# Kernel optimization log

Hardware: AMD Instinct MI355X
Metric: run time of the kernel (lower is better)

## Reference

```python
import jax, jax.numpy as jnp
import numpy as np

K = 8
D_IN = 300 + K   # 308
H = 100          # hidden size hardcoded throughout the module
N = 768          # num_words (words in one table)


def setup_inputs() -> dict:
    key = jax.random.key(0)
    ks = jax.random.split(key, 24)
    f32 = jnp.float32

    def rn(k, shape, scale=0.05):
        return jax.random.normal(k, shape, dtype=f32) * scale

    inp = {
        'vv': jax.random.normal(ks[0], (N, D_IN), dtype=f32),
        'indices': jax.random.randint(ks[1], (N, 5), 0, N),
        'indices_not_found': jax.random.randint(ks[2], (N,), 0, 2).astype(bool),
        'num_words': N,
        # ModuleA: Linear(308, 100) + tanh
        'A_W': rn(ks[3], (D_IN, H)), 'A_b': jnp.zeros((H,), f32),
        # ModuleB: consumes concat(ww[N,500], hh[N,100]) -> Linear(600,100)+tanh
        'B_W': rn(ks[4], (5 * H + H, H)), 'B_b': jnp.zeros((H,), f32),
        # ModuleB2(100,100,100): two heads, oo and new hidden hh
        'B2_Wo': rn(ks[5], (H, H)), 'B2_bo': jnp.zeros((H,), f32),
        'B2_Wh': rn(ks[6], (H, H)), 'B2_bh': jnp.zeros((H,), f32),
        # ModuleD(100,100)
        'D_W': rn(ks[7], (H, H)), 'D_b': jnp.zeros((H,), f32),
    }
    # Three ModuleAssociate2 heads (rows/cols/cells): pairwise 2-layer MLP
    # score(o_i, o_j) = Linear(H,2)(relu(Linear(2H,H)(concat(o_i,o_j))))
    for i, name in enumerate(['rows', 'cols', 'cells']):
        k1, k2 = jax.random.split(ks[8 + i])
        inp[name + '_W1'] = rn(k1, (2 * H, H))
        inp[name + '_b1'] = jnp.zeros((H,), f32)
        inp[name + '_W2'] = rn(k2, (H, 2))
        inp[name + '_b2'] = jnp.zeros((2,), f32)
    return inp


def _concat_neighbors(uu, indices, not_found):
    # gather 5 neighbor feature rows -> (N, 5*H); zero rows where not found
    y = uu[indices].reshape(indices.shape[0], 5 * uu.shape[1])  # (N,5,H)->(N,500)
    return jnp.where(not_found[:, None], 0.0, y)


def _associate(o, W1, b1, W2, b2):
    # pairwise MLP over all (i,j) pairs without materializing the 2H concat:
    # concat(o_i,o_j) @ W1 == o_i @ W1[:H] + o_j @ W1[H:]
    h = o.shape[1]
    hl = o @ W1[:h]   # (N,H)
    hr = o @ W1[h:]   # (N,H)
    hid = jax.nn.relu(hl[:, None, :] + hr[None, :, :] + b1)  # (N,N,H)
    return hid @ W2 + b2  # (N,N,2)


def reference(indices, indices_not_found, vv, num_words,
              A_W, A_b, B_W, B_b, B2_Wo, B2_bo, B2_Wh, B2_bh, D_W, D_b,
              rows_W1, rows_b1, rows_W2, rows_b2,
              cols_W1, cols_b1, cols_W2, cols_b2,
              cells_W1, cells_b1, cells_W2, cells_b2):
    iterations = 1
    uu = jnp.tanh(vv @ A_W + A_b)                 # ModuleA: (N,100)
    hh = jnp.zeros((num_words, H), vv.dtype)
    for _ in range(iterations):
        ww = _concat_neighbors(uu, indices, indices_not_found)  # (N,500)
        bb = jnp.tanh(jnp.concatenate([ww, hh], axis=1) @ B_W + B_b)  # ModuleB
        oo = jnp.tanh(bb @ B2_Wo + B2_bo)          # ModuleB2 output head
        hh = jnp.tanh(bb @ B2_Wh + B2_bh)          # ModuleB2 hidden head
        uu = jnp.tanh(hh @ D_W + D_b)              # ModuleD
    return (_associate(oo, rows_W1, rows_b1, rows_W2, rows_b2),
            _associate(oo, cols_W1, cols_b1, cols_W2, cols_b2),
            _associate(oo, cells_W1, cells_b1, cells_W2, cells_b2))
```

## Files before the change

kernel.cpp:

```cpp
#include <hip/hip_runtime.h>
#include <hip/hip_bf16.h>

#define NW   768
#define HID  100
#define DIN  308
#define RPB  2
#define TP   32
#define LDP  108

typedef const float* fp;

__global__ __launch_bounds__(512) void k_uu(fp vv, fp A_W, fp A_b,
                                            float* __restrict__ uu) {
    __shared__ float vs[RPB][DIN];
    __shared__ float part[4][RPB][128];
    const int i0 = blockIdx.x * RPB;
    for (int t = threadIdx.x; t < RPB * DIN; t += 512) {
        const int r = t / DIN, k = t % DIN;
        vs[r][k] = vv[(i0 + r) * DIN + k];
    }
    __syncthreads();
    const int c = threadIdx.x & 127;
    const int s = threadIdx.x >> 7;
    float a0 = 0.f, a1 = 0.f;
    if (c < HID) {
        const int k0 = s * 77;
#pragma unroll 11
        for (int k = k0; k < k0 + 77; ++k) {
            const float w = A_W[k * HID + c];
            a0 = fmaf(vs[0][k], w, a0);
            a1 = fmaf(vs[1][k], w, a1);
        }
    }
    part[s][0][c] = a0; part[s][1][c] = a1;
    __syncthreads();
    for (int t = threadIdx.x; t < RPB * HID; t += 512) {
        const int r = t / HID, cc = t % HID;
        float acc = A_b[cc];
#pragma unroll
        for (int s2 = 0; s2 < 4; ++s2) acc += part[s2][r][cc];
        uu[(i0 + r) * HID + cc] = tanhf(acc);
    }
}

__global__ __launch_bounds__(640) void k_fused(
    const float* __restrict__ uu, const int* __restrict__ indices,
    const int* __restrict__ nf,
    fp B_W, fp B_b, fp B2_Wo, fp B2_bo,
    fp W1r, fp b1r, fp W1c, fp b1c, fp W1e, fp b1e,
    float* __restrict__ hlhr) {
    __shared__ __align__(16) float ww[RPB][5 * HID];
    __shared__ float part[5][RPB][128];
    __shared__ __align__(16) float bbs[RPB][HID];
    __shared__ __align__(16) float oos[RPB][HID];
    __shared__ int flags[6];
    __shared__ int smode[2];

    if (threadIdx.x < 6) flags[threadIdx.x] = 0;
    __syncthreads();
    if (threadIdx.x < 192) {
        const int t = threadIdx.x;
        const unsigned vn = (unsigned)nf[t];
        if (vn > 1u) atomicOr(&flags[0], 1);
        if (vn & 0xFEFEFEFEu) atomicOr(&flags[1], 1);
        if ((t & 1) && vn) atomicOr(&flags[2], 1);
        if (!(t & 1) && vn) atomicOr(&flags[3], 1);
        const unsigned vi = (unsigned)indices[t];
        if ((t & 1) && vi) atomicOr(&flags[4], 1);
        if (!(t & 1) && vi) atomicOr(&flags[5], 1);
    }
    __syncthreads();
    if (threadIdx.x == 0) {
        int m = 0;
        if (!flags[1] && flags[0]) m = 1;
        else if (!flags[2] && flags[3]) m = 2;
        smode[0] = m;
        smode[1] = (!flags[4] && flags[5]) ? 1 : 0;
    }
    __syncthreads();
    const int mnf = smode[0], midx = smode[1];

    const int i0 = blockIdx.x * RPB;
    for (int t = threadIdx.x; t < RPB * 5 * HID; t += 640) {
        const int r = t / (5 * HID), u = t % (5 * HID);
        const int i = i0 + r;
        const bool notf = (mnf == 1) ? (((const unsigned char*)nf)[i] != 0)
                        : (mnf == 2) ? (nf[2 * i] != 0)
                                     : (nf[i] != 0);
        const int q = u / HID, cc = u % HID;
        int j = midx ? indices[2 * (i * 5 + q)] : indices[i * 5 + q];
        j = (j < 0) ? 0 : ((j >= NW) ? NW - 1 : j);
        ww[r][u] = notf ? 0.f : uu[j * HID + cc];
    }
    __syncthreads();

    const int c = threadIdx.x % 128;
    const int s = threadIdx.x / 128;

    {
        float a0 = 0.f, a1 = 0.f;
        if (c < HID) {
            const int k0 = s * 100;
#pragma unroll 5
            for (int k = k0; k < k0 + 100; k += 4) {
                const float4 w0 = *(const float4*)&ww[0][k];
                const float4 w1 = *(const float4*)&ww[1][k];
                const float b0 = B_W[(k + 0) * HID + c];
                const float b1v = B_W[(k + 1) * HID + c];
                const float b2v = B_W[(k + 2) * HID + c];
                const float b3 = B_W[(k + 3) * HID + c];
                a0 = fmaf(w0.x, b0, a0); a1 = fmaf(w1.x, b0, a1);
                a0 = fmaf(w0.y, b1v, a0); a1 = fmaf(w1.y, b1v, a1);
                a0 = fmaf(w0.z, b2v, a0); a1 = fmaf(w1.z, b2v, a1);
                a0 = fmaf(w0.w, b3, a0); a1 = fmaf(w1.w, b3, a1);
            }
        }
        part[s][0][c] = a0; part[s][1][c] = a1;
    }
    __syncthreads();
    for (int t = threadIdx.x; t < RPB * HID; t += 640) {
        const int r = t / HID, cc = t % HID;
        float acc = B_b[cc];
#pragma unroll
        for (int s2 = 0; s2 < 5; ++s2) acc += part[s2][r][cc];
        bbs[r][cc] = tanhf(acc);
    }
    __syncthreads();

    {
        float a0 = 0.f, a1 = 0.f;
        if (c < HID) {
            const int k0 = s * 20;
#pragma unroll 5
            for (int k = k0; k < k0 + 20; k += 4) {
                const float4 w0 = *(const float4*)&bbs[0][k];
                const float4 w1 = *(const float4*)&bbs[1][k];
                const float b0 = B2_Wo[(k + 0) * HID + c];
                const float b1v = B2_Wo[(k + 1) * HID + c];
                const float b2v = B2_Wo[(k + 2) * HID + c];
                const float b3 = B2_Wo[(k + 3) * HID + c];
                a0 = fmaf(w0.x, b0, a0); a1 = fmaf(w1.x, b0, a1);
                a0 = fmaf(w0.y, b1v, a0); a1 = fmaf(w1.y, b1v, a1);
                a0 = fmaf(w0.z, b2v, a0); a1 = fmaf(w1.z, b2v, a1);
                a0 = fmaf(w0.w, b3, a0); a1 = fmaf(w1.w, b3, a1);
            }
        }
        part[s][0][c] = a0; part[s][1][c] = a1;
    }
    __syncthreads();
    for (int t = threadIdx.x; t < RPB * HID; t += 640) {
        const int r = t / HID, cc = t % HID;
        float acc = B2_bo[cc];
#pragma unroll
        for (int s2 = 0; s2 < 5; ++s2) acc += part[s2][r][cc];
        oos[r][cc] = tanhf(acc);
    }
    __syncthreads();

    const int u = threadIdx.x;
    if (u < 600) {
        const int ho = u / HID;
        const int cc = u % HID;
        const int h = ho >> 1, half = ho & 1;
        fp W1 = (h == 0) ? W1r : ((h == 1) ? W1c : W1e);
        fp b1 = (h == 0) ? b1r : ((h == 1) ? b1c : b1e);
        const float bias = half ? 0.f : b1[cc];
        float a0 = bias, a1 = bias;
        const float* Wp = W1 + half * HID * HID;
#pragma unroll 5
        for (int k = 0; k < HID; k += 4) {
            const float4 o0 = *(const float4*)&oos[0][k];
            const float4 o1 = *(const float4*)&oos[1][k];
            const float b0 = Wp[(k + 0) * HID + cc];
            const float b1v = Wp[(k + 1) * HID + cc];
            const float b2v = Wp[(k + 2) * HID + cc];
            const float b3 = Wp[(k + 3) * HID + cc];
            a0 = fmaf(o0.x, b0, a0); a1 = fmaf(o1.x, b0, a1);
            a0 = fmaf(o0.y, b1v, a0); a1 = fmaf(o1.y, b1v, a1);
            a0 = fmaf(o0.z, b2v, a0); a1 = fmaf(o1.z, b2v, a1);
            a0 = fmaf(o0.w, b3, a0); a1 = fmaf(o1.w, b3, a1);
        }
        hlhr[(size_t)ho * (NW * HID) + (size_t)(i0 + 0) * HID + cc] = a0;
        hlhr[(size_t)ho * (NW * HID) + (size_t)(i0 + 1) * HID + cc] = a1;
    }
}

__global__ __launch_bounds__(256, 4) void k_pair(
    const float* __restrict__ hlhr,
    fp W2r, fp b2r, fp W2c, fp b2c, fp W2e, fp b2e,
    float* __restrict__ out) {
    __shared__ __align__(16) float hlS[TP][LDP];
    __shared__ __align__(16) float hrS[TP][LDP];
    __shared__ __align__(16) float w2a[HID];
    __shared__ __align__(16) float w2b[HID];

    const int h  = blockIdx.z;
    const int i0 = blockIdx.y * TP;
    const int j0 = blockIdx.x * TP;
    const float* hl = hlhr + (size_t)(h * 2 + 0) * (NW * HID) + (size_t)i0 * HID;
    const float* hr = hlhr + (size_t)(h * 2 + 1) * (NW * HID) + (size_t)j0 * HID;
    fp W2 = (h == 0) ? W2r : ((h == 1) ? W2c : W2e);
    fp b2 = (h == 0) ? b2r : ((h == 1) ? b2c : b2e);

    for (int t = threadIdx.x; t < TP * HID; t += 256) {
        const int r = t / HID, c = t % HID;
        hlS[r][c] = hl[t];
        hrS[r][c] = hr[t];
    }
    if (threadIdx.x < HID) {
        w2a[threadIdx.x] = W2[2 * threadIdx.x];
        w2b[threadIdx.x] = W2[2 * threadIdx.x + 1];
    }
    __syncthreads();

    const int tx = threadIdx.x & 15;
    const int ty = threadIdx.x >> 4;
    float acc0[2][2] = {};
    float acc1[2][2] = {};

#pragma unroll 5
    for (int kb = 0; kb < HID; kb += 4) {
        const float4 a0 = *(const float4*)&hlS[ty * 2 + 0][kb];
        const float4 a1 = *(const float4*)&hlS[ty * 2 + 1][kb];
        const float4 r0 = *(const float4*)&hrS[tx * 2 + 0][kb];
        const float4 r1 = *(const float4*)&hrS[tx * 2 + 1][kb];
        const float4 wa = *(const float4*)&w2a[kb];
        const float4 wb = *(const float4*)&w2b[kb];
#define STEP(cmp)                                                              \
        {                                                                      \
            const float h00 = fmaxf(a0.cmp + r0.cmp, 0.f);                     \
            const float h01 = fmaxf(a0.cmp + r1.cmp, 0.f);                     \
            const float h10 = fmaxf(a1.cmp + r0.cmp, 0.f);                     \
            const float h11 = fmaxf(a1.cmp + r1.cmp, 0.f);                     \
            acc0[0][0] = fmaf(h00, wa.cmp, acc0[0][0]);                        \
            acc1[0][0] = fmaf(h00, wb.cmp, acc1[0][0]);                        \
            acc0[0][1] = fmaf(h01, wa.cmp, acc0[0][1]);                        \
            acc1[0][1] = fmaf(h01, wb.cmp, acc1[0][1]);                        \
            acc0[1][0] = fmaf(h10, wa.cmp, acc0[1][0]);                        \
            acc1[1][0] = fmaf(h10, wb.cmp, acc1[1][0]);                        \
            acc0[1][1] = fmaf(h11, wa.cmp, acc0[1][1]);                        \
            acc1[1][1] = fmaf(h11, wb.cmp, acc1[1][1]);                        \
        }
        STEP(x) STEP(y) STEP(z) STEP(w)
#undef STEP
    }

    const float b20 = b2[0];
    const float b21 = b2[1];
#pragma unroll
    for (int ii = 0; ii < 2; ++ii) {
        const int i = i0 + ty * 2 + ii;
        const size_t rowo = ((size_t)(h * NW + i) * NW + j0 + tx * 2) * 2;
        float4 v;
        v.x = acc0[ii][0] + b20; v.y = acc1[ii][0] + b21;
        v.z = acc0[ii][1] + b20; v.w = acc1[ii][1] + b21;
        *reinterpret_cast<float4*>(out + rowo) = v;
    }
}

extern "C" void kernel_launch(void* const* d_in, const int* in_sizes, int n_in,
                              void* d_out, int out_size, void* d_ws,
                              size_t ws_size, hipStream_t stream) {
    int i_vv = -1, i_idx = -1, i_nf = -1, i_AW = -1, i_BW = -1;
    int tens[3] = {-1, -1, -1}; int n10 = 0;
    int w1s[3]  = {-1, -1, -1}; int n20 = 0;
    int w2s_[3] = {-1, -1, -1}; int n200 = 0;
    int b100[8] = {-1, -1, -1, -1, -1, -1, -1, -1}; int nb = 0;
    int b2s[3]  = {-1, -1, -1}; int nb2 = 0;
    for (int i = 0; i < n_in; ++i) {
        switch (in_sizes[i]) {
            case 236544: i_vv = i; break;
            case 3840:   i_idx = i; break;
            case 768:    i_nf = i; break;
            case 30800:  i_AW = i; break;
            case 60000:  i_BW = i; break;
            case 10000:  if (n10 < 3) tens[n10++] = i; break;
            case 20000:  if (n20 < 3) w1s[n20++] = i; break;
            case 200:    if (n200 < 3) w2s_[n200++] = i; break;
            case 100:    if (nb < 8) b100[nb++] = i; break;
            case 2:      if (nb2 < 3) b2s[nb2++] = i; break;
            default: break;
        }
    }
    fp vv          = (fp)d_in[i_vv];
    const int* idx = (const int*)d_in[i_idx];
    const int* nf  = (const int*)d_in[i_nf];
    fp A_W = (fp)d_in[i_AW],      A_b   = (fp)d_in[b100[0]];
    fp B_W = (fp)d_in[i_BW],      B_b   = (fp)d_in[b100[1]];
    fp B2_Wo = (fp)d_in[tens[0]], B2_bo = (fp)d_in[b100[2]];
    fp W1r = (fp)d_in[w1s[0]], b1r = (fp)d_in[b100[5]];
    fp W1c = (fp)d_in[w1s[1]], b1c = (fp)d_in[b100[6]];
    fp W1e = (fp)d_in[w1s[2]], b1e = (fp)d_in[b100[7]];
    fp W2r = (fp)d_in[w2s_[0]], b2r = (fp)d_in[b2s[0]];
    fp W2c = (fp)d_in[w2s_[1]], b2c = (fp)d_in[b2s[1]];
    fp W2e = (fp)d_in[w2s_[2]], b2e = (fp)d_in[b2s[2]];

    float* out = (float*)d_out;

    float* ws   = (float*)d_ws;
    float* uu   = ws;
    float* hlhr = ws + NW * HID;

    k_uu<<<NW / RPB, 512, 0, stream>>>(vv, A_W, A_b, uu);
    k_fused<<<NW / RPB, 640, 0, stream>>>(uu, idx, nf, B_W, B_b,
                                          B2_Wo, B2_bo,
                                          W1r, b1r, W1c, b1c, W1e, b1e, hlhr);
    dim3 grid(NW / TP, NW / TP, 3);
    k_pair<<<grid, 256, 0, stream>>>(hlhr, W2r, b2r, W2c, b2c, W2e, b2e, out);
}
```

Baseline: 50.13 us.

## Fuse three kernels into one persistent kernel with grid-wide atomic barriers

Merges the uu, fused MLP and pairwise kernels into a single 432-block persistent kernel, separated by two software grid barriers built on agent-scope atomics and a memset of the counters. This removes two kernel launch gaps. It also changes the pair stage tiling to 64x64 tiles with 8 outputs per thread instead of 32x32 with 4, and rebalances the reduction splits for 512 threads. It adds the risk of a deadlock if all 432 blocks are not co-resident, and the cost of spin-wait barriers plus an extra memset launch.

```diff
diff --git a/kernel.cpp b/kernel.cpp
--- a/kernel.cpp
+++ b/kernel.cpp
@@ -5,256 +5,281 @@
 #define HID  100
 #define DIN  308
 #define RPB  2
-#define TP   32
+#define NBLK 432
+#define NTHR 512
 #define LDP  108
 
 typedef const float* fp;
 
-__global__ __launch_bounds__(512) void k_uu(fp vv, fp A_W, fp A_b,
-                                            float* __restrict__ uu) {
-    __shared__ float vs[RPB][DIN];
-    __shared__ float part[4][RPB][128];
-    const int i0 = blockIdx.x * RPB;
-    for (int t = threadIdx.x; t < RPB * DIN; t += 512) {
-        const int r = t / DIN, k = t % DIN;
-        vs[r][k] = vv[(i0 + r) * DIN + k];
-    }
-    __syncthreads();
-    const int c = threadIdx.x & 127;
-    const int s = threadIdx.x >> 7;
-    float a0 = 0.f, a1 = 0.f;
-    if (c < HID) {
-        const int k0 = s * 77;
-#pragma unroll 11
-        for (int k = k0; k < k0 + 77; ++k) {
-            const float w = A_W[k * HID + c];
-            a0 = fmaf(vs[0][k], w, a0);
-            a1 = fmaf(vs[1][k], w, a1);
-        }
-    }
-    part[s][0][c] = a0; part[s][1][c] = a1;
-    __syncthreads();
-    for (int t = threadIdx.x; t < RPB * HID; t += 512) {
-        const int r = t / HID, cc = t % HID;
-        float acc = A_b[cc];
-#pragma unroll
-        for (int s2 = 0; s2 < 4; ++s2) acc += part[s2][r][cc];
-        uu[(i0 + r) * HID + cc] = tanhf(acc);
-    }
-}
-
-__global__ __launch_bounds__(640) void k_fused(
-    const float* __restrict__ uu, const int* __restrict__ indices,
-    const int* __restrict__ nf,
-    fp B_W, fp B_b, fp B2_Wo, fp B2_bo,
-    fp W1r, fp b1r, fp W1c, fp b1c, fp W1e, fp b1e,
-    float* __restrict__ hlhr) {
-    __shared__ __align__(16) float ww[RPB][5 * HID];
-    __shared__ float part[5][RPB][128];
-    __shared__ __align__(16) float bbs[RPB][HID];
-    __shared__ __align__(16) float oos[RPB][HID];
-    __shared__ int flags[6];
-    __shared__ int smode[2];
-
-    if (threadIdx.x < 6) flags[threadIdx.x] = 0;
-    __syncthreads();
-    if (threadIdx.x < 192) {
-        const int t = threadIdx.x;
-        const unsigned vn = (unsigned)nf[t];
-        if (vn > 1u) atomicOr(&flags[0], 1);
-        if (vn & 0xFEFEFEFEu) atomicOr(&flags[1], 1);
-        if ((t & 1) && vn) atomicOr(&flags[2], 1);
-        if (!(t & 1) && vn) atomicOr(&flags[3], 1);
-        const unsigned vi = (unsigned)indices[t];
-        if ((t & 1) && vi) atomicOr(&flags[4], 1);
-        if (!(t & 1) && vi) atomicOr(&flags[5], 1);
-    }
+__device__ __forceinline__ void gbar(int* bar, int idx) {
     __syncthreads();
     if (threadIdx.x == 0) {
-        int m = 0;
-        if (!flags[1] && flags[0]) m = 1;
-        else if (!flags[2] && flags[3]) m = 2;
-        smode[0] = m;
-        smode[1] = (!flags[4] && flags[5]) ? 1 : 0;
+        __hip_atomic_fetch_add(&bar[idx], 1, __ATOMIC_RELEASE,
+                               __HIP_MEMORY_SCOPE_AGENT);
+        while (__hip_atomic_load(&bar[idx], __ATOMIC_RELAXED,
+                                 __HIP_MEMORY_SCOPE_AGENT) < NBLK) {
+            __builtin_amdgcn_s_sleep(8);
+        }
+        (void)__hip_atomic_load(&bar[idx], __ATOMIC_ACQUIRE,
+                                __HIP_MEMORY_SCOPE_AGENT);
     }
     __syncthreads();
-    const int mnf = smode[0], midx = smode[1];
-
-    const int i0 = blockIdx.x * RPB;
-    for (int t = threadIdx.x; t < RPB * 5 * HID; t += 640) {
-        const int r = t / (5 * HID), u = t % (5 * HID);
-        const int i = i0 + r;
-        const bool notf = (mnf == 1) ? (((const unsigned char*)nf)[i] != 0)
-                        : (mnf == 2) ? (nf[2 * i] != 0)
-                                     : (nf[i] != 0);
-        const int q = u / HID, cc = u % HID;
-        int j = midx ? indices[2 * (i * 5 + q)] : indices[i * 5 + q];
-        j = (j < 0) ? 0 : ((j >= NW) ? NW - 1 : j);
-        ww[r][u] = notf ? 0.f : uu[j * HID + cc];
-    }
-    __syncthreads();
-
-    const int c = threadIdx.x % 128;
-    const int s = threadIdx.x / 128;
-
-    {
+}
+
+__global__ __launch_bounds__(NTHR, 4) void k_all(
+    fp vv, const int* __restrict__ indices, const int* __restrict__ nf,
+    fp A_W, fp A_b, fp B_W, fp B_b, fp B2_Wo, fp B2_bo,
+    fp W1r, fp b1r, fp W1c, fp b1c, fp W1e, fp b1e,
+    fp W2r, fp b2r, fp W2c, fp b2c, fp W2e, fp b2e,
+    float* __restrict__ uu, float* __restrict__ hlhr, int* __restrict__ bar,
+    float* __restrict__ out) {
+    __shared__ __align__(16) float smem[14032];
+    const int bid = blockIdx.x;
+    const int tid = threadIdx.x;
+
+    if (bid < NW / RPB) {
+        float (*vs)[DIN]        = (float(*)[DIN])smem;
+        float (*part)[RPB][128] = (float(*)[RPB][128])(smem + 616);
+        const int i0 = bid * RPB;
+        for (int t = tid; t < RPB * DIN; t += NTHR) {
+            const int r = t / DIN, k = t % DIN;
+            vs[r][k] = vv[(i0 + r) * DIN + k];
+        }
+        __syncthreads();
+        const int c = tid & 127;
+        const int s = tid >> 7;
         float a0 = 0.f, a1 = 0.f;
         if (c < HID) {
-            const int k0 = s * 100;
+            const int k0 = s * 77;
+#pragma unroll 11
+            for (int k = k0; k < k0 + 77; ++k) {
+                const float w = A_W[k * HID + c];
+                a0 = fmaf(vs[0][k], w, a0);
+                a1 = fmaf(vs[1][k], w, a1);
+            }
+        }
+        part[s][0][c] = a0; part[s][1][c] = a1;
+        __syncthreads();
+        for (int t = tid; t < RPB * HID; t += NTHR) {
+            const int r = t / HID, cc = t % HID;
+            float acc = A_b[cc];
+#pragma unroll
+            for (int s2 = 0; s2 < 4; ++s2) acc += part[s2][r][cc];
+            uu[(i0 + r) * HID + cc] = tanhf(acc);
+        }
+    }
+    gbar(bar, 0);
+
+    if (bid < NW / RPB) {
+        float (*ww)[500]        = (float(*)[500])smem;
+        float (*part)[RPB][128] = (float(*)[RPB][128])(smem + 1000);
+        float (*bbs)[HID]       = (float(*)[HID])(smem + 2024);
+        float (*oos)[HID]       = (float(*)[HID])(smem + 2224);
+        int*  flags             = (int*)(smem + 14024);
+
+        if (tid < 8) flags[tid] = 0;
+        __syncthreads();
+        if (tid < 192) {
+            const int t = tid;
+            const unsigned vn = (unsigned)nf[t];
+            if (vn > 1u) atomicOr(&flags[0], 1);
+            if (vn & 0xFEFEFEFEu) atomicOr(&flags[1], 1);
+            if ((t & 1) && vn) atomicOr(&flags[2], 1);
+            if (!(t & 1) && vn) atomicOr(&flags[3], 1);
+            const unsigned vi = (unsigned)indices[t];
+            if ((t & 1) && vi) atomicOr(&flags[4], 1);
+            if (!(t & 1) && vi) atomicOr(&flags[5], 1);
+        }
+        __syncthreads();
+        if (tid == 0) {
+            int m = 0;
+            if (!flags[1] && flags[0]) m = 1;
+            else if (!flags[2] && flags[3]) m = 2;
+            flags[6] = m;
+            flags[7] = (!flags[4] && flags[5]) ? 1 : 0;
+        }
+        __syncthreads();
+        const int mnf = flags[6], midx = flags[7];
+
+        const int i0 = bid * RPB;
+        for (int t = tid; t < RPB * 5 * HID; t += NTHR) {
+            const int r = t / (5 * HID), u = t % (5 * HID);
+            const int i = i0 + r;
+            const bool notf = (mnf == 1) ? (((const unsigned char*)nf)[i] != 0)
+                            : (mnf == 2) ? (nf[2 * i] != 0)
+                                         : (nf[i] != 0);
+            const int q = u / HID, cc = u % HID;
+            int j = midx ? indices[2 * (i * 5 + q)] : indices[i * 5 + q];
+            j = (j < 0) ? 0 : ((j >= NW) ? NW - 1 : j);
+            ww[r][u] = notf ? 0.f : uu[j * HID + cc];
+        }
+        __syncthreads();
+
+        const int c = tid & 127;
+        const int s = tid >> 7;
+
+        {
+            float a0 = 0.f, a1 = 0.f;
+            if (c < HID) {
+                const int k0 = s * 128;
+                const int k1 = (s < 3) ? k0 + 128 : 500;
+                for (int k = k0; k < k1; k += 4) {
+                    const float4 w0 = *(const float4*)&ww[0][k];
+                    const float4 w1 = *(const float4*)&ww[1][k];
+                    const float b0 = B_W[(k + 0) * HID + c];
+                    const float b1v = B_W[(k + 1) * HID + c];
+                    const float b2v = B_W[(k + 2) * HID + c];
+                    const float b3 = B_W[(k + 3) * HID + c];
+                    a0 = fmaf(w0.x, b0, a0); a1 = fmaf(w1.x, b0, a1);
+                    a0 = fmaf(w0.y, b1v, a0); a1 = fmaf(w1.y, b1v, a1);
+                    a0 = fmaf(w0.z, b2v, a0); a1 = fmaf(w1.z, b2v, a1);
+                    a0 = fmaf(w0.w, b3, a0); a1 = fmaf(w1.w, b3, a1);
+                }
+            }
+            part[s][0][c] = a0; part[s][1][c] = a1;
+        }
+        __syncthreads();
+        for (int t = tid; t < RPB * HID; t += NTHR) {
+            const int r = t / HID, cc = t % HID;
+            float acc = B_b[cc];
+#pragma unroll
+            for (int s2 = 0; s2 < 4; ++s2) acc += part[s2][r][cc];
+            bbs[r][cc] = tanhf(acc);
+        }
+        __syncthreads();
+
+        {
+            float a0 = 0.f, a1 = 0.f;
+            if (c < HID) {
+                const int k0 = s * 28;
+                const int k1 = (s < 3) ? k0 + 28 : 100;
+                for (int k = k0; k < k1; k += 4) {
+                    const float4 w0 = *(const float4*)&bbs[0][k];
+                    const float4 w1 = *(const float4*)&bbs[1][k];
+                    const float b0 = B2_Wo[(k + 0) * HID + c];
+                    const float b1v = B2_Wo[(k + 1) * HID + c];
+                    const float b2v = B2_Wo[(k + 2) * HID + c];
+                    const float b3 = B2_Wo[(k + 3) * HID + c];
+                    a0 = fmaf(w0.x, b0, a0); a1 = fmaf(w1.x, b0, a1);
+                    a0 = fmaf(w0.y, b1v, a0); a1 = fmaf(w1.y, b1v, a1);
+                    a0 = fmaf(w0.z, b2v, a0); a1 = fmaf(w1.z, b2v, a1);
+                    a0 = fmaf(w0.w, b3, a0); a1 = fmaf(w1.w, b3, a1);
+                }
+            }
+            part[s][0][c] = a0; part[s][1][c] = a1;
+        }
+        __syncthreads();
+        for (int t = tid; t < RPB * HID; t += NTHR) {
+            const int r = t / HID, cc = t % HID;
+            float acc = B2_bo[cc];
+#pragma unroll
+            for (int s2 = 0; s2 < 4; ++s2) acc += part[s2][r][cc];
+            oos[r][cc] = tanhf(acc);
+        }
+        __syncthreads();
+
+        for (int u = tid; u < 600; u += NTHR) {
+            const int ho = u / HID;
+            const int cc = u % HID;
+            const int h = ho >> 1, half = ho & 1;
+            fp W1 = (h == 0) ? W1r : ((h == 1) ? W1c : W1e);
+            fp b1 = (h == 0) ? b1r : ((h == 1) ? b1c : b1e);
+            const float bias = half ? 0.f : b1[cc];
+            float a0 = bias, a1 = bias;
+            const float* Wp = W1 + half * HID * HID;
 #pragma unroll 5
-            for (int k = k0; k < k0 + 100; k += 4) {
-                const float4 w0 = *(const float4*)&ww[0][k];
-                const float4 w1 = *(const float4*)&ww[1][k];
-                const float b0 = B_W[(k + 0) * HID + c];
-                const float b1v = B_W[(k + 1) * HID + c];
-                const float b2v = B_W[(k + 2) * HID + c];
-                const float b3 = B_W[(k + 3) * HID + c];
-                a0 = fmaf(w0.x, b0, a0); a1 = fmaf(w1.x, b0, a1);
-                a0 = fmaf(w0.y, b1v, a0); a1 = fmaf(w1.y, b1v, a1);
-                a0 = fmaf(w0.z, b2v, a0); a1 = fmaf(w1.z, b2v, a1);
-                a0 = fmaf(w0.w, b3, a0); a1 = fmaf(w1.w, b3, a1);
-            }
-        }
-        part[s][0][c] = a0; part[s][1][c] = a1;
-    }
-    __syncthreads();
-    for (int t = threadIdx.x; t < RPB * HID; t += 640) {
-        const int r = t / HID, cc = t % HID;
-        float acc = B_b[cc];
-#pragma unroll
-        for (int s2 = 0; s2 < 5; ++s2) acc += part[s2][r][cc];
-        bbs[r][cc] = tanhf(acc);
-    }
-    __syncthreads();
+            for (int k = 0; k < HID; k += 4) {
+                const float4 o0 = *(const float4*)&oos[0][k];
+                const float4 o1 = *(const float4*)&oos[1][k];
+                const float b0 = Wp[(k + 0) * HID + cc];
+                const float b1v = Wp[(k + 1) * HID + cc];
+                const float b2v = Wp[(k + 2) * HID + cc];
+                const float b3 = Wp[(k + 3) * HID + cc];
+                a0 = fmaf(o0.x, b0, a0); a1 = fmaf(o1.x, b0, a1);
+                a0 = fmaf(o0.y, b1v, a0); a1 = fmaf(o1.y, b1v, a1);
+                a0 = fmaf(o0.z, b2v, a0); a1 = fmaf(o1.z, b2v, a1);
+                a0 = fmaf(o0.w, b3, a0); a1 = fmaf(o1.w, b3, a1);
+            }
+            hlhr[(size_t)ho * (NW * HID) + (size_t)(i0 + 0) * HID + cc] = a0;
+            hlhr[(size_t)ho * (NW * HID) + (size_t)(i0 + 1) * HID + cc] = a1;
+        }
+    }
+    gbar(bar, 1);
 
     {
-        float a0 = 0.f, a1 = 0.f;
-        if (c < HID) {
-            const int k0 = s * 20;
-#pragma unroll 5
-            for (int k = k0; k < k0 + 20; k += 4) {
-                const float4 w0 = *(const float4*)&bbs[0][k];
-                const float4 w1 = *(const float4*)&bbs[1][k];
-                const float b0 = B2_Wo[(k + 0) * HID + c];
-                const float b1v = B2_Wo[(k + 1) * HID + c];
-                const float b2v = B2_Wo[(k + 2) * HID + c];
-                const float b3 = B2_Wo[(k + 3) * HID + c];
-                a0 = fmaf(w0.x, b0, a0); a1 = fmaf(w1.x, b0, a1);
-                a0 = fmaf(w0.y, b1v, a0); a1 = fmaf(w1.y, b1v, a1);
-                a0 = fmaf(w0.z, b2v, a0); a1 = fmaf(w1.z, b2v, a1);
-                a0 = fmaf(w0.w, b3, a0); a1 = fmaf(w1.w, b3, a1);
-            }
-        }
-        part[s][0][c] = a0; part[s][1][c] = a1;
-    }
-    __syncthreads();
-    for (int t = threadIdx.x; t < RPB * HID; t += 640) {
-        const int r = t / HID, cc = t % HID;
-        float acc = B2_bo[cc];
-#pragma unroll
-        for (int s2 = 0; s2 < 5; ++s2) acc += part[s2][r][cc];
-        oos[r][cc] = tanhf(acc);
-    }
-    __syncthreads();
-
-    const int u = threadIdx.x;
-    if (u < 600) {
-        const int ho = u / HID;
-        const int cc = u % HID;
-        const int h = ho >> 1, half = ho & 1;
-        fp W1 = (h == 0) ? W1r : ((h == 1) ? W1c : W1e);
-        fp b1 = (h == 0) ? b1r : ((h == 1) ? b1c : b1e);
-        const float bias = half ? 0.f : b1[cc];
-        float a0 = bias, a1 = bias;
-        const float* Wp = W1 + half * HID * HID;
-#pragma unroll 5
-        for (int k = 0; k < HID; k += 4) {
-            const float4 o0 = *(const float4*)&oos[0][k];
-            const float4 o1 = *(const float4*)&oos[1][k];
-            const float b0 = Wp[(k + 0) * HID + cc];
-            const float b1v = Wp[(k + 1) * HID + cc];
-            const float b2v = Wp[(k + 2) * HID + cc];
-            const float b3 = Wp[(k + 3) * HID + cc];
-            a0 = fmaf(o0.x, b0, a0); a1 = fmaf(o1.x, b0, a1);
-            a0 = fmaf(o0.y, b1v, a0); a1 = fmaf(o1.y, b1v, a1);
-            a0 = fmaf(o0.z, b2v, a0); a1 = fmaf(o1.z, b2v, a1);
-            a0 = fmaf(o0.w, b3, a0); a1 = fmaf(o1.w, b3, a1);
-        }
-        hlhr[(size_t)ho * (NW * HID) + (size_t)(i0 + 0) * HID + cc] = a0;
-        hlhr[(size_t)ho * (NW * HID) + (size_t)(i0 + 1) * HID + cc] = a1;
-    }
-}
-
-__global__ __launch_bounds__(256, 4) void k_pair(
-    const float* __restrict__ hlhr,
-    fp W2r, fp b2r, fp W2c, fp b2c, fp W2e, fp b2e,
-    float* __restrict__ out) {
-    __shared__ __align__(16) float hlS[TP][LDP];
-    __shared__ __align__(16) float hrS[TP][LDP];
-    __shared__ __align__(16) float w2a[HID];
-    __shared__ __align__(16) float w2b[HID];
-
-    const int h  = blockIdx.z;
-    const int i0 = blockIdx.y * TP;
-    const int j0 = blockIdx.x * TP;
-    const float* hl = hlhr + (size_t)(h * 2 + 0) * (NW * HID) + (size_t)i0 * HID;
-    const float* hr = hlhr + (size_t)(h * 2 + 1) * (NW * HID) + (size_t)j0 * HID;
-    fp W2 = (h == 0) ? W2r : ((h == 1) ? W2c : W2e);
-    fp b2 = (h == 0) ? b2r : ((h == 1) ? b2c : b2e);
-
-    for (int t = threadIdx.x; t < TP * HID; t += 256) {
-        const int r = t / HID, c = t % HID;
-        hlS[r][c] = hl[t];
-        hrS[r][c] = hr[t];
-    }
-    if (threadIdx.x < HID) {
-        w2a[threadIdx.x] = W2[2 * threadIdx.x];
-        w2b[threadIdx.x] = W2[2 * threadIdx.x + 1];
-    }
-    __syncthreads();
-
-    const int tx = threadIdx.x & 15;
-    const int ty = threadIdx.x >> 4;
-    float acc0[2][2] = {};
-    float acc1[2][2] = {};
-
-#pragma unroll 5
-    for (int kb = 0; kb < HID; kb += 4) {
-        const float4 a0 = *(const float4*)&hlS[ty * 2 + 0][kb];
-        const float4 a1 = *(const float4*)&hlS[ty * 2 + 1][kb];
-        const float4 r0 = *(const float4*)&hrS[tx * 2 + 0][kb];
-        const float4 r1 = *(const float4*)&hrS[tx * 2 + 1][kb];
-        const float4 wa = *(const float4*)&w2a[kb];
-        const float4 wb = *(const float4*)&w2b[kb];
+        float* hlS = smem;
+        float* hrS = smem + 64 * LDP;
+        float* w2a = smem + 2 * 64 * LDP;
+        float* w2b = w2a + HID;
+
+        const int h   = bid / 144;
+        const int rem = bid % 144;
+        const int i0  = (rem / 12) * 64;
+        const int j0  = (rem % 12) * 64;
+        const float* hl = hlhr + (size_t)(h * 2 + 0) * (NW * HID) + (size_t)i0 * HID;
+        const float* hr = hlhr + (size_t)(h * 2 + 1) * (NW * HID) + (size_t)j0 * HID;
+        fp W2 = (h == 0) ? W2r : ((h == 1) ? W2c : W2e);
+        fp b2 = (h == 0) ? b2r : ((h == 1) ? b2c : b2e);
+
+        for (int t = tid; t < 64 * HID; t += NTHR) {
+            const int r = t / HID, c = t % HID;
+            hlS[r * LDP + c] = hl[t];
+            hrS[r * LDP + c] = hr[t];
+        }
+        if (tid < HID) {
+            w2a[tid] = W2[2 * tid];
+            w2b[tid] = W2[2 * tid + 1];
+        }
+        __syncthreads();
+
+        const int tx = tid & 15;
+        const int ty = tid >> 4;
+        float acc0[2][4] = {};
+        float acc1[2][4] = {};
+
+        for (int kb = 0; kb < HID; kb += 4) {
+            const float4 a0 = *(const float4*)&hlS[(ty * 2 + 0) * LDP + kb];
+            const float4 a1 = *(const float4*)&hlS[(ty * 2 + 1) * LDP + kb];
+            const float4 r0 = *(const float4*)&hrS[(tx +  0) * LDP + kb];
+            const float4 r1 = *(const float4*)&hrS[(tx + 16) * LDP + kb];
+            const float4 r2 = *(const float4*)&hrS[(tx + 32) * LDP + kb];
+            const float4 r3 = *(const float4*)&hrS[(tx + 48) * LDP + kb];
+            const float4 wa = *(const float4*)&w2a[kb];
+            const float4 wb = *(const float4*)&w2b[kb];
 #define STEP(cmp)                                                              \
-        {                                                                      \
-            const float h00 = fmaxf(a0.cmp + r0.cmp, 0.f);                     \
-            const float h01 = fmaxf(a0.cmp + r1.cmp, 0.f);                     \
-            const float h10 = fmaxf(a1.cmp + r0.cmp, 0.f);                     \
-            const float h11 = fmaxf(a1.cmp + r1.cmp, 0.f);                     \
-            acc0[0][0] = fmaf(h00, wa.cmp, acc0[0][0]);                        \
-            acc1[0][0] = fmaf(h00, wb.cmp, acc1[0][0]);                        \
-            acc0[0][1] = fmaf(h01, wa.cmp, acc0[0][1]);                        \
-            acc1[0][1] = fmaf(h01, wb.cmp, acc1[0][1]);                        \
-            acc0[1][0] = fmaf(h10, wa.cmp, acc0[1][0]);                        \
-            acc1[1][0] = fmaf(h10, wb.cmp, acc1[1][0]);                        \
-            acc0[1][1] = fmaf(h11, wa.cmp, acc0[1][1]);                        \
-            acc1[1][1] = fmaf(h11, wb.cmp, acc1[1][1]);                        \
-        }
-        STEP(x) STEP(y) STEP(z) STEP(w)
+            {                                                                  \
+                const float av0 = a0.cmp, av1 = a1.cmp;                        \
+                const float rv[4] = {r0.cmp, r1.cmp, r2.cmp, r3.cmp};          \
+                const float wav = wa.cmp, wbv = wb.cmp;                        \
+                _Pragma("unroll")                                              \
+                for (int g = 0; g < 4; ++g) {                                  \
+                    const float h0 = fmaxf(av0 + rv[g], 0.f);                  \
+                    const float h1 = fmaxf(av1 + rv[g], 0.f);                  \
+                    acc0[0][g] = fmaf(h0, wav, acc0[0][g]);                    \
+                    acc1[0][g] = fmaf(h0, wbv, acc1[0][g]);                    \
+                    acc0[1][g] = fmaf(h1, wav, acc0[1][g]);                    \
+                    acc1[1][g] = fmaf(h1, wbv, acc1[1][g]);                    \
+                }                                                              \
+            }
+            STEP(x) STEP(y) STEP(z) STEP(w)
 #undef STEP
-    }
-
-    const float b20 = b2[0];
-    const float b21 = b2[1];
-#pragma unroll
-    for (int ii = 0; ii < 2; ++ii) {
-        const int i = i0 + ty * 2 + ii;
-        const size_t rowo = ((size_t)(h * NW + i) * NW + j0 + tx * 2) * 2;
-        float4 v;
-        v.x = acc0[ii][0] + b20; v.y = acc1[ii][0] + b21;
-        v.z = acc0[ii][1] + b20; v.w = acc1[ii][1] + b21;
-        *reinterpret_cast<float4*>(out + rowo) = v;
+        }
+
+        const float b20 = b2[0];
+        const float b21 = b2[1];
+#pragma unroll
+        for (int ii = 0; ii < 2; ++ii) {
+            const int i = i0 + ty * 2 + ii;
+#pragma unroll
+            for (int g = 0; g < 4; ++g) {
+                const int j = j0 + tx + 16 * g;
+                const size_t o = ((size_t)(h * NW + i) * NW + j) * 2;
+                float2 v;
+                v.x = acc0[ii][g] + b20;
+                v.y = acc1[ii][g] + b21;
+                *reinterpret_cast<float2*>(out + o) = v;
+            }
+        }
     }
 }
 
@@ -295,16 +320,17 @@
     fp W2c = (fp)d_in[w2s_[1]], b2c = (fp)d_in[b2s[1]];
     fp W2e = (fp)d_in[w2s_[2]], b2e = (fp)d_in[b2s[2]];
 
-    float* out = (float*)d_out;
-
+    float* out  = (float*)d_out;
     float* ws   = (float*)d_ws;
     float* uu   = ws;
     float* hlhr = ws + NW * HID;
-
-    k_uu<<<NW / RPB, 512, 0, stream>>>(vv, A_W, A_b, uu);
-    k_fused<<<NW / RPB, 640, 0, stream>>>(uu, idx, nf, B_W, B_b,
-                                          B2_Wo, B2_bo,
-                                          W1r, b1r, W1c, b1c, W1e, b1e, hlhr);
-    dim3 grid(NW / TP, NW / TP, 3);
-    k_pair<<<grid, 256, 0, stream>>>(hlhr, W2r, b2r, W2c, b2c, W2e, b2e, out);
+    int*   bar  = (int*)(ws + NW * HID + 6 * NW * HID);
+
+    hipMemsetAsync((void*)bar, 0, 2 * sizeof(int), stream);
+
+    k_all<<<NBLK, NTHR, 0, stream>>>(vv, idx, nf,
+                                     A_W, A_b, B_W, B_b, B2_Wo, B2_bo,
+                                     W1r, b1r, W1c, b1c, W1e, b1e,
+                                     W2r, b2r, W2c, b2c, W2e, b2e,
+                                     uu, hlhr, bar, out);
 }
```

Result: slower. 120.8 us (+140.9%).

## Enlarge pair-kernel tile to 64x64 with 4x4 register blocking per thread

Applied to the files above, without the earlier changes.

Changes the pairwise MLP kernel from 32x32 tiles with 2x2 outputs per thread to 64x64 tiles with 4x4 outputs per thread, using strided column assignment. The W2 weights are now read straight from global memory as float4 instead of being staged in shared memory. This raises arithmetic intensity per shared-memory load and cuts redundant tile loads. In exchange it uses more registers and shared memory (occupancy hint lowered to 2), launches fewer blocks (432), and writes float2 instead of float4.

```diff
diff --git a/kernel.cpp b/kernel.cpp
--- a/kernel.cpp
+++ b/kernel.cpp
@@ -5,7 +5,7 @@
 #define HID  100
 #define DIN  308
 #define RPB  2
-#define TP   32
+#define TQ   64
 #define LDP  108
 
 typedef const float* fp;
@@ -185,76 +185,78 @@
     }
 }
 
-__global__ __launch_bounds__(256, 4) void k_pair(
+__global__ __launch_bounds__(256, 2) void k_pair(
     const float* __restrict__ hlhr,
     fp W2r, fp b2r, fp W2c, fp b2c, fp W2e, fp b2e,
     float* __restrict__ out) {
-    __shared__ __align__(16) float hlS[TP][LDP];
-    __shared__ __align__(16) float hrS[TP][LDP];
-    __shared__ __align__(16) float w2a[HID];
-    __shared__ __align__(16) float w2b[HID];
+    __shared__ __align__(16) float hlS[TQ * LDP];
+    __shared__ __align__(16) float hrS[TQ * LDP];
 
     const int h  = blockIdx.z;
-    const int i0 = blockIdx.y * TP;
-    const int j0 = blockIdx.x * TP;
+    const int i0 = blockIdx.y * TQ;
+    const int j0 = blockIdx.x * TQ;
     const float* hl = hlhr + (size_t)(h * 2 + 0) * (NW * HID) + (size_t)i0 * HID;
     const float* hr = hlhr + (size_t)(h * 2 + 1) * (NW * HID) + (size_t)j0 * HID;
     fp W2 = (h == 0) ? W2r : ((h == 1) ? W2c : W2e);
     fp b2 = (h == 0) ? b2r : ((h == 1) ? b2c : b2e);
-
-    for (int t = threadIdx.x; t < TP * HID; t += 256) {
+    const int tid = threadIdx.x;
+
+    for (int t = tid; t < TQ * HID; t += 256) {
         const int r = t / HID, c = t % HID;
-        hlS[r][c] = hl[t];
-        hrS[r][c] = hr[t];
-    }
-    if (threadIdx.x < HID) {
-        w2a[threadIdx.x] = W2[2 * threadIdx.x];
-        w2b[threadIdx.x] = W2[2 * threadIdx.x + 1];
-    }
-    __syncthreads();
-
-    const int tx = threadIdx.x & 15;
-    const int ty = threadIdx.x >> 4;
-    float acc0[2][2] = {};
-    float acc1[2][2] = {};
-
-#pragma unroll 5
+        hlS[r * LDP + c] = hl[t];
+        hrS[r * LDP + c] = hr[t];
+    }
+    __syncthreads();
+
+    const int tx = tid & 15;
+    const int ty = tid >> 4;
+    float acc0[4][4] = {};
+    float acc1[4][4] = {};
+
     for (int kb = 0; kb < HID; kb += 4) {
-        const float4 a0 = *(const float4*)&hlS[ty * 2 + 0][kb];
-        const float4 a1 = *(const float4*)&hlS[ty * 2 + 1][kb];
-        const float4 r0 = *(const float4*)&hrS[tx * 2 + 0][kb];
-        const float4 r1 = *(const float4*)&hrS[tx * 2 + 1][kb];
-        const float4 wa = *(const float4*)&w2a[kb];
-        const float4 wb = *(const float4*)&w2b[kb];
-#define STEP(cmp)                                                              \
+        const float4 wA = *(const float4*)&W2[2 * kb];
+        const float4 wB = *(const float4*)&W2[2 * kb + 4];
+        const float4 a0 = *(const float4*)&hlS[(4 * ty + 0) * LDP + kb];
+        const float4 a1 = *(const float4*)&hlS[(4 * ty + 1) * LDP + kb];
+        const float4 a2 = *(const float4*)&hlS[(4 * ty + 2) * LDP + kb];
+        const float4 a3 = *(const float4*)&hlS[(4 * ty + 3) * LDP + kb];
+        const float4 r0 = *(const float4*)&hrS[(tx +  0) * LDP + kb];
+        const float4 r1 = *(const float4*)&hrS[(tx + 16) * LDP + kb];
+        const float4 r2 = *(const float4*)&hrS[(tx + 32) * LDP + kb];
+        const float4 r3 = *(const float4*)&hrS[(tx + 48) * LDP + kb];
+#define STEP(cmp, wa, wb)                                                      \
         {                                                                      \
-            const float h00 = fmaxf(a0.cmp + r0.cmp, 0.f);                     \
-            const float h01 = fmaxf(a0.cmp + r1.cmp, 0.f);                     \
-            const float h10 = fmaxf(a1.cmp + r0.cmp, 0.f);                     \
-            const float h11 = fmaxf(a1.cmp + r1.cmp, 0.f);                     \
-            acc0[0][0] = fmaf(h00, wa.cmp, acc0[0][0]);                        \
-            acc1[0][0] = fmaf(h00, wb.cmp, acc1[0][0]);                        \
-            acc0[0][1] = fmaf(h01, wa.cmp, acc0[0][1]);                        \
-            acc1[0][1] = fmaf(h01, wb.cmp, acc1[0][1]);                        \
-            acc0[1][0] = fmaf(h10, wa.cmp, acc0[1][0]);                        \
-            acc1[1][0] = fmaf(h10, wb.cmp, acc1[1][0]);                        \
-            acc0[1][1] = fmaf(h11, wa.cmp, acc0[1][1]);                        \
-            acc1[1][1] = fmaf(h11, wb.cmp, acc1[1][1]);                        \
-        }
-        STEP(x) STEP(y) STEP(z) STEP(w)
+            const float av[4] = {a0.cmp, a1.cmp, a2.cmp, a3.cmp};              \
+            const float rv[4] = {r0.cmp, r1.cmp, r2.cmp, r3.cmp};              \
+            _Pragma("unroll")                                                  \
+            for (int ii = 0; ii < 4; ++ii) {                                   \
+                _Pragma("unroll")                                              \
+                for (int g = 0; g < 4; ++g) {                                  \
+                    const float hv = fmaxf(av[ii] + rv[g], 0.f);               \
+                    acc0[ii][g] = fmaf(hv, wa, acc0[ii][g]);                   \
+                    acc1[ii][g] = fmaf(hv, wb, acc1[ii][g]);                   \
+                }                                                              \
+            }                                                                  \
+        }
+        STEP(x, wA.x, wA.y) STEP(y, wA.z, wA.w)
+        STEP(z, wB.x, wB.y) STEP(w, wB.z, wB.w)
 #undef STEP
     }
 
     const float b20 = b2[0];
     const float b21 = b2[1];
 #pragma unroll
-    for (int ii = 0; ii < 2; ++ii) {
-        const int i = i0 + ty * 2 + ii;
-        const size_t rowo = ((size_t)(h * NW + i) * NW + j0 + tx * 2) * 2;
-        float4 v;
-        v.x = acc0[ii][0] + b20; v.y = acc1[ii][0] + b21;
-        v.z = acc0[ii][1] + b20; v.w = acc1[ii][1] + b21;
-        *reinterpret_cast<float4*>(out + rowo) = v;
+    for (int ii = 0; ii < 4; ++ii) {
+        const int i = i0 + 4 * ty + ii;
+#pragma unroll
+        for (int g = 0; g < 4; ++g) {
+            const int j = j0 + tx + 16 * g;
+            const size_t o = ((size_t)(h * NW + i) * NW + j) * 2;
+            float2 v;
+            v.x = acc0[ii][g] + b20;
+            v.y = acc1[ii][g] + b21;
+            *reinterpret_cast<float2*>(out + o) = v;
+        }
     }
 }
 
@@ -305,6 +307,6 @@
     k_fused<<<NW / RPB, 640, 0, stream>>>(uu, idx, nf, B_W, B_b,
                                           B2_Wo, B2_bo,
                                           W1r, b1r, W1c, b1c, W1e, b1e, hlhr);
-    dim3 grid(NW / TP, NW / TP, 3);
+    dim3 grid(NW / TQ, NW / TQ, 3);
     k_pair<<<grid, 256, 0, stream>>>(hlhr, W2r, b2r, W2c, b2c, W2e, b2e, out);
 }
```

Result: slower. 51.62 us (+3.0%).

## Fuse ModuleA into gather kernel by recomputing uu for gathered neighbor rows

Applied to the files above, without the earlier changes.

Removes the separate k_uu launch and the uu workspace round-trip. Each block now loads the 10 gathered vv rows into shared memory and computes tanh(vv@A_W+b) for them directly, writing the results into ww. The cost is recomputation: each uu row is computed about five times across blocks, and each wave does a 308-long serial dot product per output column instead of splitting K across waves. It also adds about 12 KB of shared memory per block.

```diff
diff --git a/kernel.cpp b/kernel.cpp
--- a/kernel.cpp
+++ b/kernel.cpp
@@ -10,92 +10,83 @@
 
 typedef const float* fp;
 
-__global__ __launch_bounds__(512) void k_uu(fp vv, fp A_W, fp A_b,
-                                            float* __restrict__ uu) {
-    __shared__ float vs[RPB][DIN];
-    __shared__ float part[4][RPB][128];
-    const int i0 = blockIdx.x * RPB;
-    for (int t = threadIdx.x; t < RPB * DIN; t += 512) {
-        const int r = t / DIN, k = t % DIN;
-        vs[r][k] = vv[(i0 + r) * DIN + k];
-    }
-    __syncthreads();
-    const int c = threadIdx.x & 127;
-    const int s = threadIdx.x >> 7;
-    float a0 = 0.f, a1 = 0.f;
-    if (c < HID) {
-        const int k0 = s * 77;
-#pragma unroll 11
-        for (int k = k0; k < k0 + 77; ++k) {
-            const float w = A_W[k * HID + c];
-            a0 = fmaf(vs[0][k], w, a0);
-            a1 = fmaf(vs[1][k], w, a1);
-        }
-    }
-    part[s][0][c] = a0; part[s][1][c] = a1;
-    __syncthreads();
-    for (int t = threadIdx.x; t < RPB * HID; t += 512) {
-        const int r = t / HID, cc = t % HID;
-        float acc = A_b[cc];
-#pragma unroll
-        for (int s2 = 0; s2 < 4; ++s2) acc += part[s2][r][cc];
-        uu[(i0 + r) * HID + cc] = tanhf(acc);
-    }
-}
-
 __global__ __launch_bounds__(640) void k_fused(
-    const float* __restrict__ uu, const int* __restrict__ indices,
-    const int* __restrict__ nf,
-    fp B_W, fp B_b, fp B2_Wo, fp B2_bo,
+    fp vv, const int* __restrict__ indices, const int* __restrict__ nf,
+    fp A_W, fp A_b, fp B_W, fp B_b, fp B2_Wo, fp B2_bo,
     fp W1r, fp b1r, fp W1c, fp b1c, fp W1e, fp b1e,
     float* __restrict__ hlhr) {
+    __shared__ __align__(16) float vs[10][DIN];
     __shared__ __align__(16) float ww[RPB][5 * HID];
     __shared__ float part[5][RPB][128];
     __shared__ __align__(16) float bbs[RPB][HID];
     __shared__ __align__(16) float oos[RPB][HID];
-    __shared__ int flags[6];
-    __shared__ int smode[2];
-
-    if (threadIdx.x < 6) flags[threadIdx.x] = 0;
-    __syncthreads();
-    if (threadIdx.x < 192) {
-        const int t = threadIdx.x;
-        const unsigned vn = (unsigned)nf[t];
+    __shared__ int flags[8];
+    __shared__ int jrow[10];
+    __shared__ int notfv[RPB];
+    const int tid = threadIdx.x;
+    const int i0 = blockIdx.x * RPB;
+
+    if (tid < 8) flags[tid] = 0;
+    __syncthreads();
+    if (tid < 192) {
+        const unsigned vn = (unsigned)nf[tid];
         if (vn > 1u) atomicOr(&flags[0], 1);
         if (vn & 0xFEFEFEFEu) atomicOr(&flags[1], 1);
-        if ((t & 1) && vn) atomicOr(&flags[2], 1);
-        if (!(t & 1) && vn) atomicOr(&flags[3], 1);
-        const unsigned vi = (unsigned)indices[t];
-        if ((t & 1) && vi) atomicOr(&flags[4], 1);
-        if (!(t & 1) && vi) atomicOr(&flags[5], 1);
-    }
-    __syncthreads();
-    if (threadIdx.x == 0) {
+        if ((tid & 1) && vn) atomicOr(&flags[2], 1);
+        if (!(tid & 1) && vn) atomicOr(&flags[3], 1);
+        const unsigned vi = (unsigned)indices[tid];
+        if ((tid & 1) && vi) atomicOr(&flags[4], 1);
+        if (!(tid & 1) && vi) atomicOr(&flags[5], 1);
+    }
+    __syncthreads();
+    if (tid == 0) {
         int m = 0;
         if (!flags[1] && flags[0]) m = 1;
         else if (!flags[2] && flags[3]) m = 2;
-        smode[0] = m;
-        smode[1] = (!flags[4] && flags[5]) ? 1 : 0;
-    }
-    __syncthreads();
-    const int mnf = smode[0], midx = smode[1];
-
-    const int i0 = blockIdx.x * RPB;
-    for (int t = threadIdx.x; t < RPB * 5 * HID; t += 640) {
-        const int r = t / (5 * HID), u = t % (5 * HID);
+        flags[6] = m;
+        flags[7] = (!flags[4] && flags[5]) ? 1 : 0;
+    }
+    __syncthreads();
+    const int mnf = flags[6], midx = flags[7];
+
+    if (tid < 10) {
+        const int r = tid / 5, q = tid % 5;
         const int i = i0 + r;
-        const bool notf = (mnf == 1) ? (((const unsigned char*)nf)[i] != 0)
-                        : (mnf == 2) ? (nf[2 * i] != 0)
-                                     : (nf[i] != 0);
-        const int q = u / HID, cc = u % HID;
         int j = midx ? indices[2 * (i * 5 + q)] : indices[i * 5 + q];
         j = (j < 0) ? 0 : ((j >= NW) ? NW - 1 : j);
-        ww[r][u] = notf ? 0.f : uu[j * HID + cc];
-    }
-    __syncthreads();
-
-    const int c = threadIdx.x % 128;
-    const int s = threadIdx.x / 128;
+        jrow[tid] = j;
+    }
+    if (tid < RPB) {
+        const int i = i0 + tid;
+        notfv[tid] = (mnf == 1) ? (((const unsigned char*)nf)[i] != 0)
+                   : (mnf == 2) ? (nf[2 * i] != 0)
+                                : (nf[i] != 0);
+    }
+    __syncthreads();
+
+    for (int t = tid; t < 10 * DIN; t += 640) {
+        const int s = t / DIN, k = t % DIN;
+        vs[s][k] = vv[jrow[s] * DIN + k];
+    }
+    __syncthreads();
+
+    {
+        const int s = tid >> 6;
+        const int lane = tid & 63;
+        const int r = s / 5, q = s % 5;
+        const bool nz = (notfv[r] == 0);
+        for (int c = lane; c < HID; c += 64) {
+            float acc = A_b[c];
+#pragma unroll 7
+            for (int k = 0; k < DIN; ++k)
+                acc = fmaf(vs[s][k], A_W[k * HID + c], acc);
+            ww[r][q * HID + c] = nz ? tanhf(acc) : 0.f;
+        }
+    }
+    __syncthreads();
+
+    const int c = tid % 128;
+    const int s = tid / 128;
 
     {
         float a0 = 0.f, a1 = 0.f;
@@ -118,7 +109,7 @@
         part[s][0][c] = a0; part[s][1][c] = a1;
     }
     __syncthreads();
-    for (int t = threadIdx.x; t < RPB * HID; t += 640) {
+    for (int t = tid; t < RPB * HID; t += 640) {
         const int r = t / HID, cc = t % HID;
         float acc = B_b[cc];
 #pragma unroll
@@ -148,7 +139,7 @@
         part[s][0][c] = a0; part[s][1][c] = a1;
     }
     __syncthreads();
-    for (int t = threadIdx.x; t < RPB * HID; t += 640) {
+    for (int t = tid; t < RPB * HID; t += 640) {
         const int r = t / HID, cc = t % HID;
         float acc = B2_bo[cc];
 #pragma unroll
@@ -157,10 +148,9 @@
     }
     __syncthreads();
 
-    const int u = threadIdx.x;
-    if (u < 600) {
-        const int ho = u / HID;
-        const int cc = u % HID;
+    if (tid < 600) {
+        const int ho = tid / HID;
+        const int cc = tid % HID;
         const int h = ho >> 1, half = ho & 1;
         fp W1 = (h == 0) ? W1r : ((h == 1) ? W1c : W1e);
         fp b1 = (h == 0) ? b1r : ((h == 1) ? b1c : b1e);
@@ -298,11 +288,9 @@
     float* out = (float*)d_out;
 
     float* ws   = (float*)d_ws;
-    float* uu   = ws;
-    float* hlhr = ws + NW * HID;
-
-    k_uu<<<NW / RPB, 512, 0, stream>>>(vv, A_W, A_b, uu);
-    k_fused<<<NW / RPB, 640, 0, stream>>>(uu, idx, nf, B_W, B_b,
+    float* hlhr = ws;
+
+    k_fused<<<NW / RPB, 640, 0, stream>>>(vv, idx, nf, A_W, A_b, B_W, B_b,
                                           B2_Wo, B2_bo,
                                           W1r, b1r, W1c, b1c, W1e, b1e, hlhr);
     dim3 grid(NW / TP, NW / TP, 3);
```

Measured after the change: 70.54 us. 1.41x slower.
